# Kernel optimization log

Hardware: AMD Instinct MI355X
Metric: run time of the kernel (lower is better)

Reference implementation:

```python
import jax, jax.numpy as jnp
import numpy as np

D_MODEL = 1024
N_HEAD = 16
D_HEAD = D_MODEL // N_HEAD
N_CTX = 2048
ROPE_BASE = 10000.0
SCALE = 1


def _rope_cache(seq_len, d_head, dtype=jnp.float32):
    inv_freq = 1.0 / (ROPE_BASE ** (jnp.arange(0, d_head, 2, dtype=jnp.float32) / d_head))
    t = jnp.arange(seq_len, dtype=jnp.float32)
    freqs = jnp.outer(t, inv_freq)              # [S, d_head/2]
    emb = jnp.concatenate([freqs, freqs], -1)   # [S, d_head]  (concat, per source)
    cos = jnp.cos(emb)[None, :, None, :].astype(dtype)
    sin = jnp.sin(emb)[None, :, None, :].astype(dtype)
    return cos, sin


def _apply_rope(x, cos, sin):
    # x: [B, S, H, Dh]; interleaved rotate (stack then flatten), per source
    x_even = x[..., 0::2]
    x_odd = x[..., 1::2]
    x_rot = jnp.stack([-x_odd, x_even], axis=-1).reshape(x.shape)
    return x * cos + x_rot * sin


def _rmsnorm(x, w):
    eps = jnp.finfo(x.dtype).eps  # torch RMSNorm default eps
    var = jnp.mean(jnp.square(x), axis=-1, keepdims=True)
    return x * jax.lax.rsqrt(var + eps) * w


def setup_inputs() -> dict:
    key = jax.random.key(0)
    ks = jax.random.split(key, 9)
    B, S = 2, N_CTX
    x = jax.random.normal(ks[0], (B, S, D_MODEL), jnp.float32)
    s = 0.02
    Wq = jax.random.normal(ks[1], (D_MODEL, D_MODEL), jnp.float32) * s
    bq = jax.random.normal(ks[2], (D_MODEL,), jnp.float32) * s
    Wk = jax.random.normal(ks[3], (D_MODEL, D_MODEL), jnp.float32) * s
    bk = jax.random.normal(ks[4], (D_MODEL,), jnp.float32) * s
    Wv = jax.random.normal(ks[5], (D_MODEL, D_MODEL), jnp.float32) * s
    bv = jax.random.normal(ks[6], (D_MODEL,), jnp.float32) * s
    Wo = jax.random.normal(ks[7], (D_MODEL, D_MODEL), jnp.float32) * s
    norm_w = jnp.ones((D_HEAD,), jnp.float32)
    return {"x": x, "Wq": Wq, "bq": bq, "Wk": Wk, "bk": bk,
            "Wv": Wv, "bv": bv, "Wo": Wo, "norm_w": norm_w}


def reference(x, Wq, bq, Wk, bk, Wv, bv, Wo, norm_w):
    B, S, _ = x.shape
    split = lambda t: t.reshape(B, S, N_HEAD, D_HEAD)
    q = split(x @ Wq.T + bq)
    k = split(x @ Wk.T + bk)
    v = split(x @ Wv.T + bv)
    cos, sin = _rope_cache(S, D_HEAD, x.dtype)
    q = _apply_rope(_rmsnorm(q, norm_w), cos, sin)
    k = _apply_rope(_rmsnorm(k, norm_w), cos, sin)
    scores = jnp.einsum('bqhd,bkhd->bhqk', q, k)
    causal = jnp.tril(jnp.ones((S, S), x.dtype))
    pattern = jnp.square(scores / D_HEAD) * causal  # quadratic score, masked
    z = jnp.einsum('bhqk,bkhd->bqhd', pattern, v).reshape(B, S, D_MODEL)
    return x + (z @ Wo.T) * SCALE
```

## Files before the change

### kernel.cpp

```cpp
#include <hip/hip_runtime.h>
#include <math.h>


typedef float  f32x4  __attribute__((ext_vector_type(4)));
typedef short  bf16x8 __attribute__((ext_vector_type(8)));
typedef float  vf4    __attribute__((ext_vector_type(4)));
typedef unsigned short u16x4 __attribute__((ext_vector_type(4)));

static __device__ __forceinline__ unsigned short f2bf(float f) {
    union { float f; unsigned int i; } c; c.f = f;
    unsigned int x = c.i;
    return (unsigned short)((x + 0x7fffu + ((x >> 16) & 1u)) >> 16);
}
static __device__ __forceinline__ f32x4 shfl_xor4(f32x4 v, int m) {
    f32x4 r;
    r[0] = __shfl_xor(v[0], m); r[1] = __shfl_xor(v[1], m);
    r[2] = __shfl_xor(v[2], m); r[3] = __shfl_xor(v[3], m);
    return r;
}
static __device__ __forceinline__ f32x4 rsq4(f32x4 v) {
    f32x4 r;
#pragma unroll
    for (int i = 0; i < 4; i++) r[i] = rsqrtf(v[i] * (1.0f / 64.0f) + 1.1920929e-07f);
    return r;
}
static __device__ __forceinline__ void cp16(const unsigned short* g, unsigned short* l) {
    __builtin_amdgcn_global_load_lds(
        (const __attribute__((address_space(1))) unsigned int*)g,
        (__attribute__((address_space(3))) unsigned int*)l, 16, 0, 0);
}

#define FOR_2(X)  X(0) X(1)
#define FOR_M(X)  X(0) X(1) X(2) X(3)
#define FOR_MN2(X) X(0,0) X(0,1) X(0,2) X(0,3) X(1,0) X(1,1) X(1,2) X(1,3)

#define MF(c,a,b) c = __builtin_amdgcn_mfma_f32_16x16x32_bf16(a, b, c, 0, 0, 0);

__global__ __launch_bounds__(256) void cvt_all(
    const float* __restrict__ x,  const float* __restrict__ Wq,
    const float* __restrict__ Wk, const float* __restrict__ Wv,
    const float* __restrict__ Wo,
    unsigned short* __restrict__ xb,  unsigned short* __restrict__ Wqb,
    unsigned short* __restrict__ Wkb, unsigned short* __restrict__ Wvb,
    unsigned short* __restrict__ Wob, int nx4, int nw4)
{
    int i = blockIdx.x * 256 + threadIdx.x;
    const float* s; unsigned short* d; int li;
    if (i < nx4) { s = x; d = xb; li = i; }
    else {
        int idx = i - nx4;
        int r = idx / nw4; li = idx - r * nw4;
        if (r >= 4) return;
        s = (r == 0) ? Wq : (r == 1) ? Wk : (r == 2) ? Wv : Wo;
        d = (r == 0) ? Wqb : (r == 1) ? Wkb : (r == 2) ? Wvb : Wob;
    }
    vf4 v = *(const vf4*)(s + (size_t)li * 4);
    u16x4 o;
#pragma unroll
    for (int j = 0; j < 4; j++) o[j] = f2bf(v[j]);
    *(u16x4*)(d + (size_t)li * 4) = o;
}

#define SS 136

__global__ __launch_bounds__(512) void gemm_qkv(
    const unsigned short* __restrict__ xb,
    const unsigned short* __restrict__ Wqb,
    const unsigned short* __restrict__ Wkb,
    const unsigned short* __restrict__ Wvb,
    const float* __restrict__ bqf, const float* __restrict__ bkf, const float* __restrict__ bvf,
    const float* __restrict__ nwp,
    unsigned short* __restrict__ qb, unsigned short* __restrict__ kb,
    unsigned short* __restrict__ vT, int M)
{
    const int K = 1024;
    __shared__ unsigned short smem[32768];
    const int tid = threadIdx.x;
    const int n0 = blockIdx.x * 128;
    const int m0 = blockIdx.y * 128;
    const int lane = tid & 63, wid = tid >> 6;
    const int wy = wid >> 1, wx = wid & 1;
    const int l15 = lane & 15, quad = lane >> 4;
    const int r16 = lane >> 2;
    const int c8  = (lane & 3) * 8;

#define Q_DECL_ACC(mi,ni) f32x4 cq##mi##ni = {0.f,0.f,0.f,0.f}; \
                          f32x4 ck##mi##ni = {0.f,0.f,0.f,0.f}; \
                          f32x4 cv##mi##ni = {0.f,0.f,0.f,0.f};
    FOR_MN2(Q_DECL_ACC)

#define QKV_STAGE(BUF, KT) { \
        unsigned short* dstb = smem + (BUF) * 16384; \
        _Pragma("unroll") \
        for (int j = 0; j < 4; j++) { \
            const int ch = wid * 4 + j;           \
            const int mat = ch >> 3;              \
            const int row = (ch & 7) * 16 + r16; \
            const unsigned short* g = \
                (mat == 0) ? xb  + (size_t)(m0 + row) * K + (KT) + c8 : \
                (mat == 1) ? Wqb + (size_t)(n0 + row) * K + (KT) + c8 : \
                (mat == 2) ? Wkb + (size_t)(n0 + row) * K + (KT) + c8 : \
                             Wvb + (size_t)(n0 + row) * K + (KT) + c8; \
            cp16(g, &dstb[ch * 512]); \
        } }

#define QKV_COMPUTE(BUF) { \
        const unsigned short* As_  = smem + (BUF) * 16384; \
        const unsigned short* Wqs_ = As_ + 4096; \
        const unsigned short* Wks_ = As_ + 8192; \
        const unsigned short* Wvs_ = As_ + 12288; \
        const bf16x8 a0 = *(const bf16x8*)&As_[(wy * 32 +  0 + l15) * 32 + quad * 8]; \
        const bf16x8 a1 = *(const bf16x8*)&As_[(wy * 32 + 16 + l15) * 32 + quad * 8]; \
        { \
            const bf16x8 b0 = *(const bf16x8*)&Wqs_[(wx * 64 +  0 + l15) * 32 + quad * 8]; \
            const bf16x8 b1 = *(const bf16x8*)&Wqs_[(wx * 64 + 16 + l15) * 32 + quad * 8]; \
            const bf16x8 b2 = *(const bf16x8*)&Wqs_[(wx * 64 + 32 + l15) * 32 + quad * 8]; \
            const bf16x8 b3 = *(const bf16x8*)&Wqs_[(wx * 64 + 48 + l15) * 32 + quad * 8]; \
            MF(cq00,a0,b0) MF(cq01,a0,b1) MF(cq02,a0,b2) MF(cq03,a0,b3) \
            MF(cq10,a1,b0) MF(cq11,a1,b1) MF(cq12,a1,b2) MF(cq13,a1,b3) \
        } \
        { \
            const bf16x8 b0 = *(const bf16x8*)&Wks_[(wx * 64 +  0 + l15) * 32 + quad * 8]; \
            const bf16x8 b1 = *(const bf16x8*)&Wks_[(wx * 64 + 16 + l15) * 32 + quad * 8]; \
            const bf16x8 b2 = *(const bf16x8*)&Wks_[(wx * 64 + 32 + l15) * 32 + quad * 8]; \
            const bf16x8 b3 = *(const bf16x8*)&Wks_[(wx * 64 + 48 + l15) * 32 + quad * 8]; \
            MF(ck00,a0,b0) MF(ck01,a0,b1) MF(ck02,a0,b2) MF(ck03,a0,b3) \
            MF(ck10,a1,b0) MF(ck11,a1,b1) MF(ck12,a1,b2) MF(ck13,a1,b3) \
        } \
        { \
            const bf16x8 b0 = *(const bf16x8*)&Wvs_[(wx * 64 +  0 + l15) * 32 + quad * 8]; \
            const bf16x8 b1 = *(const bf16x8*)&Wvs_[(wx * 64 + 16 + l15) * 32 + quad * 8]; \
            const bf16x8 b2 = *(const bf16x8*)&Wvs_[(wx * 64 + 32 + l15) * 32 + quad * 8]; \
            const bf16x8 b3 = *(const bf16x8*)&Wvs_[(wx * 64 + 48 + l15) * 32 + quad * 8]; \
            MF(cv00,a0,b0) MF(cv01,a0,b1) MF(cv02,a0,b2) MF(cv03,a0,b3) \
            MF(cv10,a1,b0) MF(cv11,a1,b1) MF(cv12,a1,b2) MF(cv13,a1,b3) \
        } }

    QKV_STAGE(0, 0)
    __syncthreads();

    for (int kt = 0; kt < K; kt += 64) {
        QKV_STAGE(1, kt + 32)
        QKV_COMPUTE(0)
        __syncthreads();
        if (kt + 64 < K) QKV_STAGE(0, kt + 64)
        QKV_COMPUTE(1)
        __syncthreads();
    }

    const float nww0 = nwp[l15],      nww1 = nwp[16 + l15];
    const float nww2 = nwp[32 + l15], nww3 = nwp[48 + l15];
    const float lf0 = expf(-(float)l15 * 0.28782313662425572f);
    const float lf1 = expf(-(float)(l15 + 16) * 0.28782313662425572f);

#define EPI_ROPE_ONE(P,mi,ni,NW,CS,SN) { \
            float vn = P##mi##ni[r] * s2v[r] * NW; \
            float pt = __shfl_xor(vn, 1); \
            float rot = (lane & 1) ? pt : -pt; \
            smem[mrow * SS + wx * 64 + (ni) * 16 + l15] = f2bf((vn * (CS) + rot * (SN)) * 0.125f); }
#define EPI_ROPE_MI(P,mi) { f32x4 s2v = s2_##mi; \
            _Pragma("unroll") \
            for (int r = 0; r < 4; r++) { \
                const int mrow = wy * 32 + (mi) * 16 + quad * 4 + r; \
                const float t = (float)((m0 + mrow) & 2047); \
                const float a0 = t * lf0, a1 = t * lf1; \
                const float cs0 = cosf(a0), sn0 = sinf(a0); \
                const float cs1 = cosf(a1), sn1 = sinf(a1); \
                EPI_ROPE_ONE(P,mi,0,nww0,cs0,sn0) EPI_ROPE_ONE(P,mi,1,nww1,cs1,sn1) \
                EPI_ROPE_ONE(P,mi,2,nww2,cs0,sn0) EPI_ROPE_ONE(P,mi,3,nww3,cs1,sn1) } }

#define EPI_QK(P, BIASPTR, DSTPTR) { \
        const float bs0 = BIASPTR[n0 + wx * 64 + l15]; \
        const float bs1 = BIASPTR[n0 + wx * 64 + 16 + l15]; \
        const float bs2 = BIASPTR[n0 + wx * 64 + 32 + l15]; \
        const float bs3 = BIASPTR[n0 + wx * 64 + 48 + l15]; \
        P##00 += bs0; P##01 += bs1; P##02 += bs2; P##03 += bs3; \
        P##10 += bs0; P##11 += bs1; P##12 += bs2; P##13 += bs3; \
        f32x4 s2_0 = P##00*P##00 + P##01*P##01 + P##02*P##02 + P##03*P##03; \
        f32x4 s2_1 = P##10*P##10 + P##11*P##11 + P##12*P##12 + P##13*P##13; \
        s2_0 = s2_0 + shfl_xor4(s2_0,1); s2_0 = s2_0 + shfl_xor4(s2_0,2); \
        s2_0 = s2_0 + shfl_xor4(s2_0,4); s2_0 = s2_0 + shfl_xor4(s2_0,8); s2_0 = rsq4(s2_0); \
        s2_1 = s2_1 + shfl_xor4(s2_1,1); s2_1 = s2_1 + shfl_xor4(s2_1,2); \
        s2_1 = s2_1 + shfl_xor4(s2_1,4); s2_1 = s2_1 + shfl_xor4(s2_1,8); s2_1 = rsq4(s2_1); \
        EPI_ROPE_MI(P,0) EPI_ROPE_MI(P,1) \
        __syncthreads(); \
        _Pragma("unroll") \
        for (int it = 0; it < 4; it++) { \
            const int linear = tid + it * 512; \
            const int row = linear >> 4, cb = linear & 15; \
            *(bf16x8*)(DSTPTR + (size_t)(m0 + row) * 1024 + n0 + cb * 8) = \
                *(const bf16x8*)&smem[row * SS + cb * 8]; \
        } \
        __syncthreads(); }

    EPI_QK(cq, bqf, qb)
    EPI_QK(ck, bkf, kb)

    {
        const float bs0 = bvf[n0 + wx * 64 + l15];
        const float bs1 = bvf[n0 + wx * 64 + 16 + l15];
        const float bs2 = bvf[n0 + wx * 64 + 32 + l15];
        const float bs3 = bvf[n0 + wx * 64 + 48 + l15];
        cv00 += bs0; cv01 += bs1; cv02 += bs2; cv03 += bs3;
        cv10 += bs0; cv11 += bs1; cv12 += bs2; cv13 += bs3;
#define EPI_VST(mi,ni) { _Pragma("unroll") \
            for (int r = 0; r < 4; r++) { \
                const int mrow = wy * 32 + (mi) * 16 + quad * 4 + r; \
                smem[(wx * 64 + (ni) * 16 + l15) * SS + mrow] = f2bf(cv##mi##ni[r]); } }
        FOR_MN2(EPI_VST)
        __syncthreads();
        const int b = m0 >> 11, tok0 = m0 & 2047;
#pragma unroll
        for (int it = 0; it < 4; it++) {
            const int linear = tid + it * 512;
            const int rowd = linear >> 4, cb = linear & 15;
            const int head_g = (n0 >> 6) + (rowd >> 6);
            const int d = rowd & 63;
            *(bf16x8*)(vT + (((size_t)b * 16 + head_g) * 64 + d) * 2048 + tok0 + cb * 8) =
                *(const bf16x8*)&smem[rowd * SS + cb * 8];
        }
    }
}

__global__ __launch_bounds__(512) void gemm_out(
    const unsigned short* __restrict__ zb,
    const unsigned short* __restrict__ Wob,
    const float* __restrict__ x, float* __restrict__ out, int M)
{
    const int K = 1024;
    __shared__ unsigned short smem[16384];
    const int tid = threadIdx.x;
    const int n0 = blockIdx.x * 128;
    const int m0 = blockIdx.y * 128;
    const int lane = tid & 63, wid = tid >> 6;
    const int wy = wid >> 1, wx = wid & 1;
    const int l15 = lane & 15, quad = lane >> 4;
    const int r16 = lane >> 2;
    const int c8  = (lane & 3) * 8;

#define G_DECL_ACC(mi,ni) f32x4 c##mi##ni = {0.f, 0.f, 0.f, 0.f};
    FOR_MN2(G_DECL_ACC)

#define O_STAGE(BUF, KT) { \
        unsigned short* dstb = smem + (BUF) * 8192; \
        _Pragma("unroll") \
        for (int j = 0; j < 2; j++) { \
            const int ch = wid * 2 + j;           \
            const int mat = ch >> 3;              \
            const int row = (ch & 7) * 16 + r16; \
            const unsigned short* g = (mat == 0) \
                ? zb  + (size_t)(m0 + row) * K + (KT) + c8 \
                : Wob + (size_t)(n0 + row) * K + (KT) + c8; \
            cp16(g, &dstb[ch * 512]); \
        } }

#define O_COMPUTE(BUF) { \
        const unsigned short* As_ = smem + (BUF) * 8192; \
        const unsigned short* Ws_ = As_ + 4096; \
        const bf16x8 a0 = *(const bf16x8*)&As_[(wy * 32 +  0 + l15) * 32 + quad * 8]; \
        const bf16x8 a1 = *(const bf16x8*)&As_[(wy * 32 + 16 + l15) * 32 + quad * 8]; \
        const bf16x8 b0 = *(const bf16x8*)&Ws_[(wx * 64 +  0 + l15) * 32 + quad * 8]; \
        const bf16x8 b1 = *(const bf16x8*)&Ws_[(wx * 64 + 16 + l15) * 32 + quad * 8]; \
        const bf16x8 b2 = *(const bf16x8*)&Ws_[(wx * 64 + 32 + l15) * 32 + quad * 8]; \
        const bf16x8 b3 = *(const bf16x8*)&Ws_[(wx * 64 + 48 + l15) * 32 + quad * 8]; \
        MF(c00,a0,b0) MF(c01,a0,b1) MF(c02,a0,b2) MF(c03,a0,b3) \
        MF(c10,a1,b0) MF(c11,a1,b1) MF(c12,a1,b2) MF(c13,a1,b3) }

    O_STAGE(0, 0)
    __syncthreads();

    for (int kt = 0; kt < K; kt += 64) {
        O_STAGE(1, kt + 32)
        O_COMPUTE(0)
        __syncthreads();
        if (kt + 64 < K) O_STAGE(0, kt + 64)
        O_COMPUTE(1)
        __syncthreads();
    }

#define G_OUTST(mi,ni) { _Pragma("unroll") \
        for (int r = 0; r < 4; r++) { \
            const int m = m0 + wy * 32 + (mi) * 16 + quad * 4 + r; \
            const int n = n0 + wx * 64 + (ni) * 16 + l15; \
            out[(size_t)m * 1024 + n] = c##mi##ni[r] + x[(size_t)m * 1024 + n]; } }
    FOR_MN2(G_OUTST)
}

__global__ __launch_bounds__(256) void attn_mfma(
    const unsigned short* __restrict__ qb, const unsigned short* __restrict__ kb,
    const unsigned short* __restrict__ vT, unsigned short* __restrict__ zb)
{
    __shared__ unsigned short Qs[128 * 72];
    __shared__ unsigned short Ks[64 * 72];
    __shared__ unsigned short Vs[64 * 72];
    __shared__ unsigned short Pm[128 * 72];
    const int tid = threadIdx.x;
    const int qt = 15 - blockIdx.x;
    const int bh = blockIdx.y;
    const int b = bh >> 4, h = bh & 15;
    const int lane = tid & 63, wq = tid >> 6;
    const int l15 = lane & 15, quad = lane >> 4;
    const size_t tokbase = (size_t)b * 2048;
    const int q0 = qt * 128;

#pragma unroll
    for (int j = 0; j < 4; j++) {
        const int u = tid + j * 256;
        const int row = u >> 3, seg = (u & 7) * 8;
        bf16x8 v = *(const bf16x8*)(qb + (tokbase + q0 + row) * 1024 + h * 64 + seg);
        *(bf16x8*)&Qs[row * 72 + seg] = v;
    }
    __syncthreads();
    const bf16x8 aq00 = *(const bf16x8*)&Qs[(wq * 32 + l15) * 72 + quad * 8];
    const bf16x8 aq01 = *(const bf16x8*)&Qs[(wq * 32 + l15) * 72 + 32 + quad * 8];
    const bf16x8 aq10 = *(const bf16x8*)&Qs[(wq * 32 + 16 + l15) * 72 + quad * 8];
    const bf16x8 aq11 = *(const bf16x8*)&Qs[(wq * 32 + 16 + l15) * 72 + 32 + quad * 8];

    const int kr = tid >> 3;
    const int sg = (tid & 7) * 8;

    bf16x8 pk0, pk1, pv0, pv1;
#define A_GLB(KT) { \
        pk0 = *(const bf16x8*)(kb + (tokbase + (KT) * 64 + kr) * 1024 + h * 64 + sg); \
        pk1 = *(const bf16x8*)(kb + (tokbase + (KT) * 64 + kr + 32) * 1024 + h * 64 + sg); \
        pv0 = *(const bf16x8*)(vT + ((size_t)bh * 64 + kr) * 2048 + (KT) * 64 + sg); \
        pv1 = *(const bf16x8*)(vT + ((size_t)bh * 64 + kr + 32) * 2048 + (KT) * 64 + sg); }

#define A_DECL_Z(mi,n) f32x4 z_##mi##n = {0.f, 0.f, 0.f, 0.f};
    FOR_MN2(A_DECL_Z)

    const int nkt = 2 * qt + 2;
    A_GLB(0)
    for (int kt = 0; kt < nkt; kt++) {
        __syncthreads();
        *(bf16x8*)&Ks[kr * 72 + sg] = pk0;
        *(bf16x8*)&Ks[(kr + 32) * 72 + sg] = pk1;
        *(bf16x8*)&Vs[kr * 72 + sg] = pv0;
        *(bf16x8*)&Vs[(kr + 32) * 72 + sg] = pv1;
        __syncthreads();
        if (kt + 1 < nkt) A_GLB(kt + 1)

#define A_DECL_S(mi,n) f32x4 s_##mi##n = {0.f, 0.f, 0.f, 0.f};
        FOR_MN2(A_DECL_S)
#define A_QKH(KS, AQ0, AQ1) { \
        bf16x8 b0 = *(const bf16x8*)&Ks[(l15) * 72 + (KS) * 32 + quad * 8]; \
        bf16x8 b1 = *(const bf16x8*)&Ks[(16 + l15) * 72 + (KS) * 32 + quad * 8]; \
        bf16x8 b2 = *(const bf16x8*)&Ks[(32 + l15) * 72 + (KS) * 32 + quad * 8]; \
        bf16x8 b3 = *(const bf16x8*)&Ks[(48 + l15) * 72 + (KS) * 32 + quad * 8]; \
        s_00 = __builtin_amdgcn_mfma_f32_16x16x32_bf16(AQ0, b0, s_00, 0, 0, 0); \
        s_01 = __builtin_amdgcn_mfma_f32_16x16x32_bf16(AQ0, b1, s_01, 0, 0, 0); \
        s_02 = __builtin_amdgcn_mfma_f32_16x16x32_bf16(AQ0, b2, s_02, 0, 0, 0); \
        s_03 = __builtin_amdgcn_mfma_f32_16x16x32_bf16(AQ0, b3, s_03, 0, 0, 0); \
        s_10 = __builtin_amdgcn_mfma_f32_16x16x32_bf16(AQ1, b0, s_10, 0, 0, 0); \
        s_11 = __builtin_amdgcn_mfma_f32_16x16x32_bf16(AQ1, b1, s_11, 0, 0, 0); \
        s_12 = __builtin_amdgcn_mfma_f32_16x16x32_bf16(AQ1, b2, s_12, 0, 0, 0); \
        s_13 = __builtin_amdgcn_mfma_f32_16x16x32_bf16(AQ1, b3, s_13, 0, 0, 0); }
        A_QKH(0, aq00, aq10)
        A_QKH(1, aq01, aq11)

        const bool needmask = (kt >= 2 * qt);
#define A_PSTORE(mi,n) { \
        f32x4 p4 = s_##mi##n * s_##mi##n; \
        if (needmask) { _Pragma("unroll") \
            for (int r = 0; r < 4; r++) \
                if (kt * 64 + (n) * 16 + l15 > q0 + wq * 32 + (mi) * 16 + quad * 4 + r) p4[r] = 0.f; } \
        _Pragma("unroll") \
        for (int r = 0; r < 4; r++) \
            Pm[(wq * 32 + (mi) * 16 + quad * 4 + r) * 72 + (n) * 16 + l15] = f2bf(p4[r]); }
        FOR_MN2(A_PSTORE)

#define A_PVH(KS) { \
        bf16x8 ap0 = *(const bf16x8*)&Pm[(wq * 32 + l15) * 72 + (KS) * 32 + quad * 8]; \
        bf16x8 ap1 = *(const bf16x8*)&Pm[(wq * 32 + 16 + l15) * 72 + (KS) * 32 + quad * 8]; \
        bf16x8 u0 = *(const bf16x8*)&Vs[(l15) * 72 + (KS) * 32 + quad * 8]; \
        bf16x8 u1 = *(const bf16x8*)&Vs[(16 + l15) * 72 + (KS) * 32 + quad * 8]; \
        bf16x8 u2 = *(const bf16x8*)&Vs[(32 + l15) * 72 + (KS) * 32 + quad * 8]; \
        bf16x8 u3 = *(const bf16x8*)&Vs[(48 + l15) * 72 + (KS) * 32 + quad * 8]; \
        z_00 = __builtin_amdgcn_mfma_f32_16x16x32_bf16(ap0, u0, z_00, 0, 0, 0); \
        z_01 = __builtin_amdgcn_mfma_f32_16x16x32_bf16(ap0, u1, z_01, 0, 0, 0); \
        z_02 = __builtin_amdgcn_mfma_f32_16x16x32_bf16(ap0, u2, z_02, 0, 0, 0); \
        z_03 = __builtin_amdgcn_mfma_f32_16x16x32_bf16(ap0, u3, z_03, 0, 0, 0); \
        z_10 = __builtin_amdgcn_mfma_f32_16x16x32_bf16(ap1, u0, z_10, 0, 0, 0); \
        z_11 = __builtin_amdgcn_mfma_f32_16x16x32_bf16(ap1, u1, z_11, 0, 0, 0); \
        z_12 = __builtin_amdgcn_mfma_f32_16x16x32_bf16(ap1, u2, z_12, 0, 0, 0); \
        z_13 = __builtin_amdgcn_mfma_f32_16x16x32_bf16(ap1, u3, z_13, 0, 0, 0); }
        A_PVH(0)
        A_PVH(1)
    }

#define A_ZST(mi,n) { _Pragma("unroll") \
        for (int r = 0; r < 4; r++) \
            Pm[(wq * 32 + (mi) * 16 + quad * 4 + r) * 72 + (n) * 16 + l15] = f2bf(z_##mi##n[r]); }
    FOR_MN2(A_ZST)
#pragma unroll
    for (int it = 0; it < 4; it++) {
        const int linear = it * 64 + lane;
        const int row = linear >> 3, cb = linear & 7;
        *(bf16x8*)(zb + (tokbase + q0 + wq * 32 + row) * 1024 + h * 64 + cb * 8) =
            *(const bf16x8*)&Pm[(wq * 32 + row) * 72 + cb * 8];
    }
}

extern "C" void kernel_launch(void* const* d_in, const int* in_sizes, int n_in,
                              void* d_out, int out_size, void* d_ws, size_t ws_size,
                              hipStream_t stream)
{
    const float* x  = (const float*)d_in[0];
    const float* Wq = (const float*)d_in[1];
    const float* bq = (const float*)d_in[2];
    const float* Wk = (const float*)d_in[3];
    const float* bk = (const float*)d_in[4];
    const float* Wv = (const float*)d_in[5];
    const float* bv = (const float*)d_in[6];
    const float* Wo = (const float*)d_in[7];
    const float* nw = (const float*)d_in[8];
    float* out = (float*)d_out;

    const int D = 1024;
    const int M = in_sizes[0] / D;

    unsigned short* xbb = (unsigned short*)d_ws;
    unsigned short* Wqb = xbb + (size_t)M * D;
    unsigned short* Wkb = Wqb + (size_t)D * D;
    unsigned short* Wvb = Wkb + (size_t)D * D;
    unsigned short* Wob = Wvb + (size_t)D * D;
    unsigned short* qbw = Wob + (size_t)D * D;
    unsigned short* kbw = qbw + (size_t)M * D;
    unsigned short* vTw = kbw + (size_t)M * D;
    unsigned short* zbw = vTw + (size_t)M * D;

    const int nx4 = M * D / 4, nw4 = D * D / 4;
    const int ncvt = nx4 + 4 * nw4;
    cvt_all<<<(ncvt + 255) / 256, 256, 0, stream>>>(
        x, Wq, Wk, Wv, Wo, xbb, Wqb, Wkb, Wvb, Wob, nx4, nw4);

    gemm_qkv<<<dim3(D / 128, M / 128), 512, 0, stream>>>(
        xbb, Wqb, Wkb, Wvb, bq, bk, bv, nw, qbw, kbw, vTw, M);

    attn_mfma<<<dim3(16, (M / 2048) * 16), 256, 0, stream>>>(qbw, kbw, vTw, zbw);

    gemm_out<<<dim3(D / 128, M / 128), 512, 0, stream>>>(zbw, Wob, x, out, M);
}
```

Measured before the change: 226.7 us.

## Split fused QKV GEMM into per-projection blocks along grid z

The QKV projection kernel no longer computes Q, K and V together in each 512-thread block. It now launches a third grid dimension, one slice per projection, with 256-thread blocks in which each warp computes a 64x64 tile. This triples the block count and shrinks shared memory per block, so more blocks can be resident at once and the GPU is better filled. The cost is that each x tile is now loaded three times, and the epilogue branches on z between the RMSNorm/RoPE path and the V transpose path.

```diff
diff --git a/kernel.cpp b/kernel.cpp
--- a/kernel.cpp
+++ b/kernel.cpp
@@ -32,6 +32,8 @@
 
 #define FOR_2(X)  X(0) X(1)
 #define FOR_M(X)  X(0) X(1) X(2) X(3)
+#define FOR_MN(X) X(0,0) X(0,1) X(0,2) X(0,3) X(1,0) X(1,1) X(1,2) X(1,3) \
+                  X(2,0) X(2,1) X(2,2) X(2,3) X(3,0) X(3,1) X(3,2) X(3,3)
 #define FOR_MN2(X) X(0,0) X(0,1) X(0,2) X(0,3) X(1,0) X(1,1) X(1,2) X(1,3)
 
 #define MF(c,a,b) c = __builtin_amdgcn_mfma_f32_16x16x32_bf16(a, b, c, 0, 0, 0);
@@ -63,7 +65,7 @@
 
 #define SS 136
 
-__global__ __launch_bounds__(512) void gemm_qkv(
+__global__ __launch_bounds__(256, 3) void gemm_qkvz(
     const unsigned short* __restrict__ xb,
     const unsigned short* __restrict__ Wqb,
     const unsigned short* __restrict__ Wkb,
@@ -71,10 +73,13 @@
     const float* __restrict__ bqf, const float* __restrict__ bkf, const float* __restrict__ bvf,
     const float* __restrict__ nwp,
     unsigned short* __restrict__ qb, unsigned short* __restrict__ kb,
-    unsigned short* __restrict__ vT, int M)
+    unsigned short* __restrict__ vT)
 {
     const int K = 1024;
-    __shared__ unsigned short smem[32768];
+    __shared__ unsigned short smem[17408];
+    const int z = blockIdx.z;
+    const unsigned short* Wb = (z == 0) ? Wqb : (z == 1) ? Wkb : Wvb;
+    const float* bias = (z == 0) ? bqf : (z == 1) ? bkf : bvf;
     const int tid = threadIdx.x;
     const int n0 = blockIdx.x * 128;
     const int m0 = blockIdx.y * 128;
@@ -84,135 +89,109 @@
     const int r16 = lane >> 2;
     const int c8  = (lane & 3) * 8;
 
-#define Q_DECL_ACC(mi,ni) f32x4 cq##mi##ni = {0.f,0.f,0.f,0.f}; \
-                          f32x4 ck##mi##ni = {0.f,0.f,0.f,0.f}; \
-                          f32x4 cv##mi##ni = {0.f,0.f,0.f,0.f};
-    FOR_MN2(Q_DECL_ACC)
-
-#define QKV_STAGE(BUF, KT) { \
-        unsigned short* dstb = smem + (BUF) * 16384; \
+#define Z_DECL_ACC(mi,ni) f32x4 c##mi##ni = {0.f, 0.f, 0.f, 0.f};
+    FOR_MN(Z_DECL_ACC)
+
+#define Z_STAGE(BUF, KT) { \
+        unsigned short* dstb = smem + (BUF) * 8192; \
         _Pragma("unroll") \
         for (int j = 0; j < 4; j++) { \
             const int ch = wid * 4 + j;           \
             const int mat = ch >> 3;              \
             const int row = (ch & 7) * 16 + r16; \
-            const unsigned short* g = \
-                (mat == 0) ? xb  + (size_t)(m0 + row) * K + (KT) + c8 : \
-                (mat == 1) ? Wqb + (size_t)(n0 + row) * K + (KT) + c8 : \
-                (mat == 2) ? Wkb + (size_t)(n0 + row) * K + (KT) + c8 : \
-                             Wvb + (size_t)(n0 + row) * K + (KT) + c8; \
+            const unsigned short* g = mat \
+                ? Wb + (size_t)(n0 + row) * K + (KT) + c8 \
+                : xb + (size_t)(m0 + row) * K + (KT) + c8; \
             cp16(g, &dstb[ch * 512]); \
         } }
 
-#define QKV_COMPUTE(BUF) { \
-        const unsigned short* As_  = smem + (BUF) * 16384; \
-        const unsigned short* Wqs_ = As_ + 4096; \
-        const unsigned short* Wks_ = As_ + 8192; \
-        const unsigned short* Wvs_ = As_ + 12288; \
-        const bf16x8 a0 = *(const bf16x8*)&As_[(wy * 32 +  0 + l15) * 32 + quad * 8]; \
-        const bf16x8 a1 = *(const bf16x8*)&As_[(wy * 32 + 16 + l15) * 32 + quad * 8]; \
-        { \
-            const bf16x8 b0 = *(const bf16x8*)&Wqs_[(wx * 64 +  0 + l15) * 32 + quad * 8]; \
-            const bf16x8 b1 = *(const bf16x8*)&Wqs_[(wx * 64 + 16 + l15) * 32 + quad * 8]; \
-            const bf16x8 b2 = *(const bf16x8*)&Wqs_[(wx * 64 + 32 + l15) * 32 + quad * 8]; \
-            const bf16x8 b3 = *(const bf16x8*)&Wqs_[(wx * 64 + 48 + l15) * 32 + quad * 8]; \
-            MF(cq00,a0,b0) MF(cq01,a0,b1) MF(cq02,a0,b2) MF(cq03,a0,b3) \
-            MF(cq10,a1,b0) MF(cq11,a1,b1) MF(cq12,a1,b2) MF(cq13,a1,b3) \
-        } \
-        { \
-            const bf16x8 b0 = *(const bf16x8*)&Wks_[(wx * 64 +  0 + l15) * 32 + quad * 8]; \
-            const bf16x8 b1 = *(const bf16x8*)&Wks_[(wx * 64 + 16 + l15) * 32 + quad * 8]; \
-            const bf16x8 b2 = *(const bf16x8*)&Wks_[(wx * 64 + 32 + l15) * 32 + quad * 8]; \
-            const bf16x8 b3 = *(const bf16x8*)&Wks_[(wx * 64 + 48 + l15) * 32 + quad * 8]; \
-            MF(ck00,a0,b0) MF(ck01,a0,b1) MF(ck02,a0,b2) MF(ck03,a0,b3) \
-            MF(ck10,a1,b0) MF(ck11,a1,b1) MF(ck12,a1,b2) MF(ck13,a1,b3) \
-        } \
-        { \
-            const bf16x8 b0 = *(const bf16x8*)&Wvs_[(wx * 64 +  0 + l15) * 32 + quad * 8]; \
-            const bf16x8 b1 = *(const bf16x8*)&Wvs_[(wx * 64 + 16 + l15) * 32 + quad * 8]; \
-            const bf16x8 b2 = *(const bf16x8*)&Wvs_[(wx * 64 + 32 + l15) * 32 + quad * 8]; \
-            const bf16x8 b3 = *(const bf16x8*)&Wvs_[(wx * 64 + 48 + l15) * 32 + quad * 8]; \
-            MF(cv00,a0,b0) MF(cv01,a0,b1) MF(cv02,a0,b2) MF(cv03,a0,b3) \
-            MF(cv10,a1,b0) MF(cv11,a1,b1) MF(cv12,a1,b2) MF(cv13,a1,b3) \
-        } }
-
-    QKV_STAGE(0, 0)
+#define Z_COMPUTE(BUF) { \
+        const unsigned short* As_ = smem + (BUF) * 8192; \
+        const unsigned short* Bs_ = As_ + 4096; \
+        const bf16x8 a0 = *(const bf16x8*)&As_[(wy * 64 +  0 + l15) * 32 + quad * 8]; \
+        const bf16x8 a1 = *(const bf16x8*)&As_[(wy * 64 + 16 + l15) * 32 + quad * 8]; \
+        const bf16x8 a2 = *(const bf16x8*)&As_[(wy * 64 + 32 + l15) * 32 + quad * 8]; \
+        const bf16x8 a3 = *(const bf16x8*)&As_[(wy * 64 + 48 + l15) * 32 + quad * 8]; \
+        const bf16x8 b0 = *(const bf16x8*)&Bs_[(wx * 64 +  0 + l15) * 32 + quad * 8]; \
+        const bf16x8 b1 = *(const bf16x8*)&Bs_[(wx * 64 + 16 + l15) * 32 + quad * 8]; \
+        const bf16x8 b2 = *(const bf16x8*)&Bs_[(wx * 64 + 32 + l15) * 32 + quad * 8]; \
+        const bf16x8 b3 = *(const bf16x8*)&Bs_[(wx * 64 + 48 + l15) * 32 + quad * 8]; \
+        MF(c00,a0,b0) MF(c01,a0,b1) MF(c02,a0,b2) MF(c03,a0,b3) \
+        MF(c10,a1,b0) MF(c11,a1,b1) MF(c12,a1,b2) MF(c13,a1,b3) \
+        MF(c20,a2,b0) MF(c21,a2,b1) MF(c22,a2,b2) MF(c23,a2,b3) \
+        MF(c30,a3,b0) MF(c31,a3,b1) MF(c32,a3,b2) MF(c33,a3,b3) }
+
+    Z_STAGE(0, 0)
     __syncthreads();
 
     for (int kt = 0; kt < K; kt += 64) {
-        QKV_STAGE(1, kt + 32)
-        QKV_COMPUTE(0)
-        __syncthreads();
-        if (kt + 64 < K) QKV_STAGE(0, kt + 64)
-        QKV_COMPUTE(1)
-        __syncthreads();
-    }
-
-    const float nww0 = nwp[l15],      nww1 = nwp[16 + l15];
-    const float nww2 = nwp[32 + l15], nww3 = nwp[48 + l15];
-    const float lf0 = expf(-(float)l15 * 0.28782313662425572f);
-    const float lf1 = expf(-(float)(l15 + 16) * 0.28782313662425572f);
-
-#define EPI_ROPE_ONE(P,mi,ni,NW,CS,SN) { \
-            float vn = P##mi##ni[r] * s2v[r] * NW; \
+        Z_STAGE(1, kt + 32)
+        Z_COMPUTE(0)
+        __syncthreads();
+        if (kt + 64 < K) Z_STAGE(0, kt + 64)
+        Z_COMPUTE(1)
+        __syncthreads();
+    }
+
+    const float bs0 = bias[n0 + wx * 64 + l15];
+    const float bs1 = bias[n0 + wx * 64 + 16 + l15];
+    const float bs2 = bias[n0 + wx * 64 + 32 + l15];
+    const float bs3 = bias[n0 + wx * 64 + 48 + l15];
+#define Z_BIAS(mi) c##mi##0 += bs0; c##mi##1 += bs1; c##mi##2 += bs2; c##mi##3 += bs3;
+    FOR_M(Z_BIAS)
+
+    if (z < 2) {
+        const float nww0 = nwp[l15],      nww1 = nwp[16 + l15];
+        const float nww2 = nwp[32 + l15], nww3 = nwp[48 + l15];
+        const float lf0 = expf(-(float)l15 * 0.28782313662425572f);
+        const float lf1 = expf(-(float)(l15 + 16) * 0.28782313662425572f);
+
+#define Z_S2(mi) f32x4 s2_##mi = c##mi##0*c##mi##0 + c##mi##1*c##mi##1 + \
+                                 c##mi##2*c##mi##2 + c##mi##3*c##mi##3; \
+        s2_##mi = s2_##mi + shfl_xor4(s2_##mi, 1); \
+        s2_##mi = s2_##mi + shfl_xor4(s2_##mi, 2); \
+        s2_##mi = s2_##mi + shfl_xor4(s2_##mi, 4); \
+        s2_##mi = s2_##mi + shfl_xor4(s2_##mi, 8); \
+        s2_##mi = rsq4(s2_##mi);
+        FOR_M(Z_S2)
+
+#define Z_ROPE_ONE(mi,ni,NW,CS,SN) { \
+            float vn = c##mi##ni[r] * s2v[r] * NW; \
             float pt = __shfl_xor(vn, 1); \
             float rot = (lane & 1) ? pt : -pt; \
             smem[mrow * SS + wx * 64 + (ni) * 16 + l15] = f2bf((vn * (CS) + rot * (SN)) * 0.125f); }
-#define EPI_ROPE_MI(P,mi) { f32x4 s2v = s2_##mi; \
+#define Z_ROPE_MI(mi) { f32x4 s2v = s2_##mi; \
             _Pragma("unroll") \
             for (int r = 0; r < 4; r++) { \
-                const int mrow = wy * 32 + (mi) * 16 + quad * 4 + r; \
+                const int mrow = wy * 64 + (mi) * 16 + quad * 4 + r; \
                 const float t = (float)((m0 + mrow) & 2047); \
                 const float a0 = t * lf0, a1 = t * lf1; \
                 const float cs0 = cosf(a0), sn0 = sinf(a0); \
                 const float cs1 = cosf(a1), sn1 = sinf(a1); \
-                EPI_ROPE_ONE(P,mi,0,nww0,cs0,sn0) EPI_ROPE_ONE(P,mi,1,nww1,cs1,sn1) \
-                EPI_ROPE_ONE(P,mi,2,nww2,cs0,sn0) EPI_ROPE_ONE(P,mi,3,nww3,cs1,sn1) } }
-
-#define EPI_QK(P, BIASPTR, DSTPTR) { \
-        const float bs0 = BIASPTR[n0 + wx * 64 + l15]; \
-        const float bs1 = BIASPTR[n0 + wx * 64 + 16 + l15]; \
-        const float bs2 = BIASPTR[n0 + wx * 64 + 32 + l15]; \
-        const float bs3 = BIASPTR[n0 + wx * 64 + 48 + l15]; \
-        P##00 += bs0; P##01 += bs1; P##02 += bs2; P##03 += bs3; \
-        P##10 += bs0; P##11 += bs1; P##12 += bs2; P##13 += bs3; \
-        f32x4 s2_0 = P##00*P##00 + P##01*P##01 + P##02*P##02 + P##03*P##03; \
-        f32x4 s2_1 = P##10*P##10 + P##11*P##11 + P##12*P##12 + P##13*P##13; \
-        s2_0 = s2_0 + shfl_xor4(s2_0,1); s2_0 = s2_0 + shfl_xor4(s2_0,2); \
-        s2_0 = s2_0 + shfl_xor4(s2_0,4); s2_0 = s2_0 + shfl_xor4(s2_0,8); s2_0 = rsq4(s2_0); \
-        s2_1 = s2_1 + shfl_xor4(s2_1,1); s2_1 = s2_1 + shfl_xor4(s2_1,2); \
-        s2_1 = s2_1 + shfl_xor4(s2_1,4); s2_1 = s2_1 + shfl_xor4(s2_1,8); s2_1 = rsq4(s2_1); \
-        EPI_ROPE_MI(P,0) EPI_ROPE_MI(P,1) \
-        __syncthreads(); \
-        _Pragma("unroll") \
-        for (int it = 0; it < 4; it++) { \
-            const int linear = tid + it * 512; \
-            const int row = linear >> 4, cb = linear & 15; \
-            *(bf16x8*)(DSTPTR + (size_t)(m0 + row) * 1024 + n0 + cb * 8) = \
-                *(const bf16x8*)&smem[row * SS + cb * 8]; \
-        } \
-        __syncthreads(); }
-
-    EPI_QK(cq, bqf, qb)
-    EPI_QK(ck, bkf, kb)
-
-    {
-        const float bs0 = bvf[n0 + wx * 64 + l15];
-        const float bs1 = bvf[n0 + wx * 64 + 16 + l15];
-        const float bs2 = bvf[n0 + wx * 64 + 32 + l15];
-        const float bs3 = bvf[n0 + wx * 64 + 48 + l15];
-        cv00 += bs0; cv01 += bs1; cv02 += bs2; cv03 += bs3;
-        cv10 += bs0; cv11 += bs1; cv12 += bs2; cv13 += bs3;
-#define EPI_VST(mi,ni) { _Pragma("unroll") \
+                Z_ROPE_ONE(mi,0,nww0,cs0,sn0) Z_ROPE_ONE(mi,1,nww1,cs1,sn1) \
+                Z_ROPE_ONE(mi,2,nww2,cs0,sn0) Z_ROPE_ONE(mi,3,nww3,cs1,sn1) } }
+        FOR_M(Z_ROPE_MI)
+
+        __syncthreads();
+        unsigned short* dst = z ? kb : qb;
+#pragma unroll
+        for (int it = 0; it < 8; it++) {
+            const int linear = tid + it * 256;
+            const int row = linear >> 4, cb = linear & 15;
+            *(bf16x8*)(dst + (size_t)(m0 + row) * 1024 + n0 + cb * 8) =
+                *(const bf16x8*)&smem[row * SS + cb * 8];
+        }
+    } else {
+#define Z_VST(mi,ni) { _Pragma("unroll") \
             for (int r = 0; r < 4; r++) { \
-                const int mrow = wy * 32 + (mi) * 16 + quad * 4 + r; \
-                smem[(wx * 64 + (ni) * 16 + l15) * SS + mrow] = f2bf(cv##mi##ni[r]); } }
-        FOR_MN2(EPI_VST)
+                const int mrow = wy * 64 + (mi) * 16 + quad * 4 + r; \
+                smem[(wx * 64 + (ni) * 16 + l15) * SS + mrow] = f2bf(c##mi##ni[r]); } }
+        FOR_MN(Z_VST)
         __syncthreads();
         const int b = m0 >> 11, tok0 = m0 & 2047;
 #pragma unroll
-        for (int it = 0; it < 4; it++) {
-            const int linear = tid + it * 512;
+        for (int it = 0; it < 8; it++) {
+            const int linear = tid + it * 256;
             const int rowd = linear >> 4, cb = linear & 15;
             const int head_g = (n0 >> 6) + (rowd >> 6);
             const int d = rowd & 63;
@@ -434,8 +413,8 @@
     cvt_all<<<(ncvt + 255) / 256, 256, 0, stream>>>(
         x, Wq, Wk, Wv, Wo, xbb, Wqb, Wkb, Wvb, Wob, nx4, nw4);
 
-    gemm_qkv<<<dim3(D / 128, M / 128), 512, 0, stream>>>(
-        xbb, Wqb, Wkb, Wvb, bq, bk, bv, nw, qbw, kbw, vTw, M);
+    gemm_qkvz<<<dim3(D / 128, M / 128, 3), 256, 0, stream>>>(
+        xbb, Wqb, Wkb, Wvb, bq, bk, bv, nw, qbw, kbw, vTw);
 
     attn_mfma<<<dim3(16, (M / 2048) * 16), 256, 0, stream>>>(qbw, kbw, vTw, zbw);
 
```

New measurement: 211.6 us. 6.7% less time.
